# Kernel optimization log

Hardware: AMD Instinct MI355X
Metric: run time of the kernel (lower is better)

Reference implementation:

```python
import jax, jax.numpy as jnp
import numpy as np

B, C, L = 8, 512, 4096
KC, VC, H = 512, 512, 8
DK, DV = KC // H, VC // H
EPS = 1e-5


def _ln(x, g, b):
    m = jnp.mean(x, axis=-1, keepdims=True)
    v = jnp.var(x, axis=-1, keepdims=True)
    return (x - m) * jax.lax.rsqrt(v + EPS) * g + b


def setup_inputs() -> dict:
    key = jax.random.key(0)
    ks = jax.random.split(key, 12)
    s = 0.02
    return {
        "z1": jax.random.normal(ks[0], (B, C, L), jnp.float32),
        "z2": jax.random.normal(ks[1], (B, C, L), jnp.float32),
        "Wq": jax.random.normal(ks[2], (KC, C), jnp.float32) * s,
        "bq": jnp.zeros((KC,), jnp.float32),
        "Wk": jax.random.normal(ks[3], (KC, C), jnp.float32) * s,
        "bk": jnp.zeros((KC,), jnp.float32),
        "Wv": jax.random.normal(ks[4], (VC, C), jnp.float32) * s,
        "bv": jnp.zeros((VC,), jnp.float32),
        "Wr": jax.random.normal(ks[5], (C, VC), jnp.float32) * s,
        "br": jnp.zeros((C,), jnp.float32),
        "g1": jnp.ones((C,), jnp.float32),
        "be1": jnp.zeros((C,), jnp.float32),
        "W1": jax.random.normal(ks[6], (2 * C, C), jnp.float32) * s,
        "b1": jnp.zeros((2 * C,), jnp.float32),
        "W2": jax.random.normal(ks[7], (C, 2 * C), jnp.float32) * s,
        "b2": jnp.zeros((C,), jnp.float32),
        "g2": jnp.ones((C,), jnp.float32),
        "be2": jnp.zeros((C,), jnp.float32),
    }


def reference(z1, z2, Wq, bq, Wk, bk, Wv, bv, Wr, br, g1, be1, W1, b1, W2, b2, g2, be2):
    # 1x1 Conv1d projections (channels-first)
    q = jnp.einsum('oc,bcl->bol', Wq, z1) + bq[None, :, None]
    k = jnp.einsum('oc,bcl->bol', Wk, z2) + bk[None, :, None]
    v = jnp.einsum('oc,bcl->bol', Wv, z2) + bv[None, :, None]
    qh = q.reshape(B, H, DK, L)
    kh = k.reshape(B, H, DK, L)
    vh = v.reshape(B, H, DV, L)
    # efficient attention: keys softmax over length, queries over channels
    kh = jax.nn.softmax(kh, axis=-1)
    qh = jax.nn.softmax(qh, axis=2)
    ctx = jnp.einsum('bhkl,bhvl->bhkv', kh, vh)          # [B,H,DK,DV]
    att = jnp.einsum('bhkv,bhkl->bhvl', ctx, qh)          # [B,H,DV,L]
    att = att.reshape(B, VC, L)
    z = jnp.einsum('oc,bcl->bol', Wr, att) + br[None, :, None] + z1  # reprojection + residual
    # b c l -> b l c, LayerNorm, FFN, back
    x = z.transpose(0, 2, 1)
    x = _ln(x, g1, be1)
    h = jax.nn.elu(x @ W1.T + b1)
    y = h @ W2.T + b2
    y = _ln(y, g2, be2)
    return y.transpose(0, 2, 1)
```

## Files before the change

kernel.cpp:

```cpp
#include <hip/hip_runtime.h>
#include <math.h>

#define B_   8
#define C_   512
#define L_   4096
#define H_   8
#define DK_  64
#define C2_  1024

typedef unsigned short ushort;
typedef short     bf16x8_t __attribute__((ext_vector_type(8)));
typedef float     f32x4_t  __attribute__((ext_vector_type(4)));
typedef unsigned short u16x8 __attribute__((ext_vector_type(8)));
typedef unsigned short u16x4 __attribute__((ext_vector_type(4)));

__device__ __forceinline__ float bf2f(ushort u) {
    unsigned int x = ((unsigned int)u) << 16;
    float f; __builtin_memcpy(&f, &x, 4); return f;
}
__device__ __forceinline__ ushort f2bf(float f) {
    unsigned int x; __builtin_memcpy(&x, &f, 4);
    x = (x + 0x7FFFu + ((x >> 16) & 1u)) >> 16;
    return (ushort)x;
}

#define GLOAD_LDS16(gp, lp) \
    __builtin_amdgcn_global_load_lds((const __attribute__((address_space(1))) void*)(gp), \
                                     (__attribute__((address_space(3))) void*)(lp), 16, 0, 0)

__global__ __launch_bounds__(256) void transpose_in(const float* __restrict__ in,
                                                    ushort* __restrict__ out)
{
    const int b = blockIdx.z, c0 = blockIdx.y * 64, l0 = blockIdx.x * 64;
    __shared__ float t[64][65];
    const int tid = threadIdx.x;
    {
        const int c = tid >> 4, l4 = (tid & 15) * 4;
        const float* ip = in + ((size_t)b * C_ + c0) * L_ + l0;
#pragma unroll
        for (int cc = c; cc < 64; cc += 16) {
            float4 v = *(const float4*)(ip + (size_t)cc * L_ + l4);
            t[l4 + 0][cc] = v.x; t[l4 + 1][cc] = v.y;
            t[l4 + 2][cc] = v.z; t[l4 + 3][cc] = v.w;
        }
    }
    __syncthreads();
    {
        const int l = tid >> 3, c8 = (tid & 7) * 8;
        ushort* op = out + ((size_t)b * L_ + l0) * C_ + c0;
#pragma unroll
        for (int ll = l; ll < 64; ll += 32) {
            u16x8 v;
#pragma unroll
            for (int i = 0; i < 8; ++i) v[i] = f2bf(t[ll][c8 + i]);
            *(u16x8*)(op + (size_t)ll * C_ + c8) = v;
        }
    }
}

__global__ __launch_bounds__(256) void transpose_out(const float* __restrict__ in,
                                                     float* __restrict__ out)
{
    const int b = blockIdx.z, c0 = blockIdx.y * 64, l0 = blockIdx.x * 64;
    __shared__ float t[64][65];
    const int tid = threadIdx.x;
    {
        const int l = tid >> 4, c4 = (tid & 15) * 4;
#pragma unroll
        for (int ll = l; ll < 64; ll += 16) {
            float4 v = *(const float4*)(in + ((size_t)(b * L_ + l0 + ll)) * C_ + c0 + c4);
            t[c4 + 0][ll] = v.x; t[c4 + 1][ll] = v.y;
            t[c4 + 2][ll] = v.z; t[c4 + 3][ll] = v.w;
        }
    }
    __syncthreads();
    {
        const int c = tid >> 4, l4 = (tid & 15) * 4;
        float* op = out + ((size_t)b * C_ + c0) * L_ + l0;
#pragma unroll
        for (int cc = c; cc < 64; cc += 16) {
            float4 v = {t[cc][l4], t[cc][l4 + 1], t[cc][l4 + 2], t[cc][l4 + 3]};
            *(float4*)(op + (size_t)cc * L_ + l4) = v;
        }
    }
}

__global__ __launch_bounds__(256) void cvt_bf16(const float* __restrict__ in,
                                                ushort* __restrict__ out, int n4)
{
    const int i = blockIdx.x * 256 + threadIdx.x;
    if (i < n4) {
        float4 v = *(const float4*)(in + 4 * (size_t)i);
        u16x4 o; o[0] = f2bf(v.x); o[1] = f2bf(v.y); o[2] = f2bf(v.z); o[3] = f2bf(v.w);
        *(u16x4*)(out + 4 * (size_t)i) = o;
    }
}

__global__ __launch_bounds__(256) void zero_kernel(float* __restrict__ p, int n4)
{
    const int i = blockIdx.x * 256 + threadIdx.x;
    if (i < n4) { float4 z = {0.f, 0.f, 0.f, 0.f}; *(float4*)(p + 4 * (size_t)i) = z; }
}

template<int ACT, bool HAS_RES>
__global__ __launch_bounds__(512, 2) void conv_mfma(
    const ushort* __restrict__ A, const ushort* __restrict__ Wt,
    const float* __restrict__ bias, const ushort* __restrict__ res,
    ushort* __restrict__ out, int M, int N, int K)
{
    const int m0 = blockIdx.x * 256;
    const int n0 = blockIdx.y * 256;
    const int tid = threadIdx.x;
    const int w = tid >> 6, lane = tid & 63;
    const int wm = (w >> 2) * 128, wn = (w & 3) * 64;
    const int l16 = lane & 15, quad = lane >> 4;

    __shared__ ushort smem[32768];

    const int sRow = tid >> 2;
    const int sSwz = ((tid & 3) ^ (sRow & 3)) * 8;
    const ushort* gA0 = A  + (size_t)(m0 + sRow) * K + sSwz;
    const ushort* gA1 = A  + (size_t)(m0 + 128 + sRow) * K + sSwz;
    const ushort* gB0 = Wt + (size_t)(n0 + sRow) * K + sSwz;
    const ushort* gB1 = Wt + (size_t)(n0 + 128 + sRow) * K + sSwz;
    const int dA0 = (w * 16) * 32;
    const int dA1 = (128 + w * 16) * 32;

    f32x4_t acc[8][4];
#pragma unroll
    for (int i = 0; i < 8; ++i)
#pragma unroll
        for (int j = 0; j < 4; ++j) acc[i][j] = (f32x4_t){0.f, 0.f, 0.f, 0.f};

    const int nt = K >> 5;

    {
        ushort* bufA = smem;
        ushort* bufB = smem + 8192;
        GLOAD_LDS16(gA0, bufA + dA0);
        GLOAD_LDS16(gA1, bufA + dA1);
        GLOAD_LDS16(gB0, bufB + dA0);
        GLOAD_LDS16(gB1, bufB + dA1);
    }

    for (int t = 0; t < nt; ++t) {
        const ushort* bufA = smem + (t & 1) * 16384;
        const ushort* bufB = bufA + 8192;
        __builtin_amdgcn_s_barrier();
        asm volatile("" ::: "memory");
        if (t + 1 < nt) {
            ushort* nA = smem + ((t + 1) & 1) * 16384;
            ushort* nB = nA + 8192;
            const size_t co = (size_t)(t + 1) * 32;
            GLOAD_LDS16(gA0 + co, nA + dA0);
            GLOAD_LDS16(gA1 + co, nA + dA1);
            GLOAD_LDS16(gB0 + co, nB + dA0);
            GLOAD_LDS16(gB1 + co, nB + dA1);
            asm volatile("s_waitcnt vmcnt(4)" ::: "memory");
        } else {
            asm volatile("s_waitcnt vmcnt(0)" ::: "memory");
        }
        __builtin_amdgcn_s_barrier();
        asm volatile("" ::: "memory");

        bf16x8_t wf[4];
#pragma unroll
        for (int j = 0; j < 4; ++j) {
            const int br = wn + j * 16 + l16;
            wf[j] = *(const bf16x8_t*)(bufB + br * 32 + (quad ^ (br & 3)) * 8);
        }
        __builtin_amdgcn_s_setprio(1);
#pragma unroll
        for (int i = 0; i < 8; ++i) {
            const int ar = wm + i * 16 + l16;
            const bf16x8_t af = *(const bf16x8_t*)(bufA + ar * 32 + (quad ^ (ar & 3)) * 8);
#pragma unroll
            for (int j = 0; j < 4; ++j)
                acc[i][j] = __builtin_amdgcn_mfma_f32_16x16x32_bf16(wf[j], af, acc[i][j], 0, 0, 0);
        }
        __builtin_amdgcn_s_setprio(0);
    }

#pragma unroll
    for (int j = 0; j < 4; ++j) {
        const int nb = n0 + wn + j * 16 + quad * 4;
        const float4 bo = *(const float4*)(bias + nb);
        const float bv[4] = {bo.x, bo.y, bo.z, bo.w};
#pragma unroll
        for (int i = 0; i < 8; ++i) {
            const int m = m0 + wm + i * 16 + l16;
            float v[4];
#pragma unroll
            for (int r = 0; r < 4; ++r) v[r] = acc[i][j][r] + bv[r];
            if (HAS_RES) {
                const u16x4 rv = *(const u16x4*)(res + (size_t)m * N + nb);
#pragma unroll
                for (int r = 0; r < 4; ++r) v[r] += bf2f(rv[r]);
            }
            if (ACT == 1) {
#pragma unroll
                for (int r = 0; r < 4; ++r) v[r] = (v[r] > 0.f) ? v[r] : (__expf(v[r]) - 1.f);
            }
            u16x4 pv;
#pragma unroll
            for (int r = 0; r < 4; ++r) pv[r] = f2bf(v[r]);
            *(u16x4*)(out + (size_t)m * N + nb) = pv;
        }
    }
}

__global__ __launch_bounds__(256) void kstat_chunk(const ushort* __restrict__ k,
                                                   float2* __restrict__ stats)
{
    const int cg = blockIdx.x;
    const int bc = blockIdx.y;
    const int b = bc >> 3, ch = bc & 7;
    const int tid = threadIdx.x;
    const int g = tid & 7;
    const int kk = tid >> 3;
    const int w = tid >> 6, lane = tid & 63;
    const ushort* base = k + ((size_t)(b * L_) + ch * 512) * C_ + cg * 64 + g * 8;

    __shared__ float red[4][8][8];
    __shared__ float mcol[64];

    float fm[8];
#pragma unroll
    for (int i = 0; i < 8; ++i) fm[i] = -3.0e38f;
    for (int r = kk; r < 512; r += 32) {
        u16x8 v = *(const u16x8*)(base + (size_t)r * C_);
#pragma unroll
        for (int i = 0; i < 8; ++i) fm[i] = fmaxf(fm[i], bf2f(v[i]));
    }
#pragma unroll
    for (int off = 8; off <= 32; off <<= 1)
#pragma unroll
        for (int i = 0; i < 8; ++i) fm[i] = fmaxf(fm[i], __shfl_xor(fm[i], off));
    if ((lane >> 3) == 0)
#pragma unroll
        for (int i = 0; i < 8; ++i) red[w][g][i] = fm[i];
    __syncthreads();
    if (tid < 64) {
        const int g2 = tid >> 3, j = tid & 7;
        mcol[g2 * 8 + j] = fmaxf(fmaxf(red[0][g2][j], red[1][g2][j]),
                                 fmaxf(red[2][g2][j], red[3][g2][j]));
    }
    __syncthreads();
    float fmc[8];
#pragma unroll
    for (int i = 0; i < 8; ++i) fmc[i] = mcol[g * 8 + i];

    float fs[8] = {};
    for (int r = kk; r < 512; r += 32) {
        u16x8 v = *(const u16x8*)(base + (size_t)r * C_);
#pragma unroll
        for (int i = 0; i < 8; ++i) fs[i] += __expf(bf2f(v[i]) - fmc[i]);
    }
#pragma unroll
    for (int off = 8; off <= 32; off <<= 1)
#pragma unroll
        for (int i = 0; i < 8; ++i) fs[i] += __shfl_xor(fs[i], off);
    __syncthreads();
    if ((lane >> 3) == 0)
#pragma unroll
        for (int i = 0; i < 8; ++i) red[w][g][i] = fs[i];
    __syncthreads();
    if (tid < 64) {
        const int g2 = tid >> 3, j = tid & 7;
        const float s = red[0][g2][j] + red[1][g2][j] + red[2][g2][j] + red[3][g2][j];
        const int c = cg * 64 + g2 * 8 + j;
        stats[((size_t)(b * C_ + c)) * 8 + ch] = make_float2(mcol[g2 * 8 + j], s);
    }
}

__global__ __launch_bounds__(256) void kstat_merge(const float2* __restrict__ stats,
                                                   float2* __restrict__ minv)
{
    const int i = blockIdx.x * 256 + threadIdx.x;
    if (i >= B_ * C_) return;
    float2 st[8];
    float m = -3.0e38f;
#pragma unroll
    for (int ch = 0; ch < 8; ++ch) { st[ch] = stats[(size_t)i * 8 + ch]; m = fmaxf(m, st[ch].x); }
    float s = 0.f;
#pragma unroll
    for (int ch = 0; ch < 8; ++ch) s += st[ch].y * __expf(st[ch].x - m);
    minv[i] = make_float2(m, 1.f / s);
}

__global__ __launch_bounds__(256) void ctx_mfma(
    const ushort* __restrict__ kk, const ushort* __restrict__ vv,
    const float2* __restrict__ minv, float* __restrict__ ctx)
{
    const int bh = blockIdx.y, b = bh >> 3, h = bh & 7;
    const int l0 = blockIdx.x * 256;
    const int tid = threadIdx.x, w = tid >> 6, lane = tid & 63;
    const int l16 = lane & 15, quad = lane >> 4;

    __shared__ ushort sK[64 * 72];
    __shared__ ushort sV[64 * 72];

    const int grp = tid >> 7;
    const int st  = tid & 127;
    const int sc8 = (st & 7) * 8;
    const int sl4 = (st >> 3) * 4;
    const ushort* gsrc = (grp ? vv : kk)
        + ((size_t)(b * L_ + l0 + sl4)) * C_ + h * 64 + sc8;
    ushort* dst = grp ? sV : sK;

    float2 cst[8];
#pragma unroll
    for (int i = 0; i < 8; ++i)
        cst[i] = minv[(size_t)b * C_ + h * 64 + sc8 + i];

    f32x4_t acc[4];
#pragma unroll
    for (int j = 0; j < 4; ++j) acc[j] = (f32x4_t){0.f, 0.f, 0.f, 0.f};

    for (int tile = 0; tile < 4; ++tile) {
        u16x8 vr[4];
#pragma unroll
        for (int j = 0; j < 4; ++j)
            vr[j] = *(const u16x8*)(gsrc + ((size_t)(tile * 64 + j)) * C_);
        __syncthreads();
        if (grp == 0) {
#pragma unroll
            for (int c = 0; c < 8; ++c) {
                u16x4 o;
#pragma unroll
                for (int j = 0; j < 4; ++j)
                    o[j] = f2bf(__expf(bf2f(vr[j][c]) - cst[c].x) * cst[c].y);
                *(u16x4*)(dst + (sc8 + c) * 72 + sl4) = o;
            }
        } else {
#pragma unroll
            for (int c = 0; c < 8; ++c) {
                u16x4 o;
#pragma unroll
                for (int j = 0; j < 4; ++j) o[j] = vr[j][c];
                *(u16x4*)(dst + (sc8 + c) * 72 + sl4) = o;
            }
        }
        __syncthreads();
#pragma unroll
        for (int k0 = 0; k0 < 64; k0 += 32) {
            const bf16x8_t vf = *(const bf16x8_t*)(sV + (w * 16 + l16) * 72 + k0 + quad * 8);
#pragma unroll
            for (int j = 0; j < 4; ++j) {
                const bf16x8_t kf = *(const bf16x8_t*)(sK + (j * 16 + l16) * 72 + k0 + quad * 8);
                acc[j] = __builtin_amdgcn_mfma_f32_16x16x32_bf16(vf, kf, acc[j], 0, 0, 0);
            }
        }
    }
    float* cp = ctx + (size_t)bh * 4096;
#pragma unroll
    for (int j = 0; j < 4; ++j)
#pragma unroll
        for (int r = 0; r < 4; ++r)
            atomicAdd(&cp[(w * 16 + quad * 4 + r) * 64 + (j * 16 + l16)], acc[j][r]);
}

__global__ __launch_bounds__(256) void att_mfma(
    const ushort* __restrict__ q, const float* __restrict__ ctx,
    ushort* __restrict__ att)
{
    const int bh = blockIdx.y, b = bh >> 3, h = bh & 7;
    const int l0 = blockIdx.x * 128;
    const int tid = threadIdx.x, w = tid >> 6, lane = tid & 63;
    const int l16 = lane & 15, quad = lane >> 4;

    __shared__ ushort sQ[128 * 72];
    __shared__ ushort sC[64 * 72];

    {
        const int part = tid & 7;
#pragma unroll
        for (int rr = tid >> 3; rr < 128; rr += 32) {
            u16x8 v = *(const u16x8*)(q + ((size_t)(b * L_ + l0 + rr)) * C_ + h * 64 + part * 8);
            float f[8], m = -3.0e38f;
#pragma unroll
            for (int i = 0; i < 8; ++i) { f[i] = bf2f(v[i]); m = fmaxf(m, f[i]); }
            m = fmaxf(m, __shfl_xor(m, 1));
            m = fmaxf(m, __shfl_xor(m, 2));
            m = fmaxf(m, __shfl_xor(m, 4));
            float s = 0.f;
#pragma unroll
            for (int i = 0; i < 8; ++i) { f[i] = __expf(f[i] - m); s += f[i]; }
            s += __shfl_xor(s, 1); s += __shfl_xor(s, 2); s += __shfl_xor(s, 4);
            const float inv = 1.f / s;
            u16x8 o;
#pragma unroll
            for (int i = 0; i < 8; ++i) o[i] = f2bf(f[i] * inv);
            *(u16x8*)(sQ + rr * 72 + part * 8) = o;
        }
        const int dv = tid >> 2, dk0 = (tid & 3) * 16;
        const float* cp = ctx + (size_t)bh * 4096 + dv * 64 + dk0;
#pragma unroll
        for (int i = 0; i < 16; ++i) sC[dv * 72 + dk0 + i] = f2bf(cp[i]);
    }
    __syncthreads();

    f32x4_t acc[2][4];
#pragma unroll
    for (int i = 0; i < 2; ++i)
#pragma unroll
        for (int j = 0; j < 4; ++j) acc[i][j] = (f32x4_t){0.f, 0.f, 0.f, 0.f};

#pragma unroll
    for (int ks = 0; ks < 2; ++ks) {
        const int k0 = ks * 32;
        bf16x8_t aq[2], bc[4];
#pragma unroll
        for (int i = 0; i < 2; ++i)
            aq[i] = *(const bf16x8_t*)(sQ + (w * 32 + i * 16 + l16) * 72 + k0 + quad * 8);
#pragma unroll
        for (int j = 0; j < 4; ++j)
            bc[j] = *(const bf16x8_t*)(sC + (j * 16 + l16) * 72 + k0 + quad * 8);
#pragma unroll
        for (int i = 0; i < 2; ++i)
#pragma unroll
            for (int j = 0; j < 4; ++j)
                acc[i][j] = __builtin_amdgcn_mfma_f32_16x16x32_bf16(aq[i], bc[j], acc[i][j], 0, 0, 0);
    }

#pragma unroll
    for (int j = 0; j < 4; ++j)
#pragma unroll
        for (int i = 0; i < 2; ++i) {
            const int mb = l0 + w * 32 + i * 16 + quad * 4;
#pragma unroll
            for (int r = 0; r < 4; ++r)
                att[((size_t)(b * L_ + mb + r)) * C_ + h * 64 + j * 16 + l16] = f2bf(acc[i][j][r]);
        }
}

template<bool OUTF32>
__global__ __launch_bounds__(256) void ln_row(
    const ushort* __restrict__ in, const float* __restrict__ g,
    const float* __restrict__ be, ushort* __restrict__ outb,
    float* __restrict__ outf)
{
    const int tid = threadIdx.x, w = tid >> 6, lane = tid & 63;
    const size_t row = (size_t)blockIdx.x * 4 + w;
    const ushort* p = in + row * C_ + lane * 8;
    u16x8 v = *(const u16x8*)p;
    float f[8], s = 0.f, s2 = 0.f;
#pragma unroll
    for (int i = 0; i < 8; ++i) { f[i] = bf2f(v[i]); s += f[i]; s2 = fmaf(f[i], f[i], s2); }
#pragma unroll
    for (int o = 1; o < 64; o <<= 1) { s += __shfl_xor(s, o); s2 += __shfl_xor(s2, o); }
    const float mean = s * (1.f / C_);
    const float var  = s2 * (1.f / C_) - mean * mean;
    const float inv  = rsqrtf(var + 1e-5f);
    if (OUTF32) {
        float* op = outf + row * C_ + lane * 8;
#pragma unroll
        for (int i = 0; i < 8; ++i)
            op[i] = (f[i] - mean) * inv * g[lane * 8 + i] + be[lane * 8 + i];
    } else {
        u16x8 ov;
#pragma unroll
        for (int i = 0; i < 8; ++i)
            ov[i] = f2bf((f[i] - mean) * inv * g[lane * 8 + i] + be[lane * 8 + i]);
        *(u16x8*)(outb + row * C_ + lane * 8) = ov;
    }
}

extern "C" void kernel_launch(void* const* d_in, const int* in_sizes, int n_in,
                              void* d_out, int out_size, void* d_ws, size_t ws_size,
                              hipStream_t stream)
{
    const float* z1  = (const float*)d_in[0];
    const float* z2  = (const float*)d_in[1];
    const float* Wq  = (const float*)d_in[2];
    const float* bq  = (const float*)d_in[3];
    const float* Wk  = (const float*)d_in[4];
    const float* bk  = (const float*)d_in[5];
    const float* Wv  = (const float*)d_in[6];
    const float* bv  = (const float*)d_in[7];
    const float* Wr  = (const float*)d_in[8];
    const float* br  = (const float*)d_in[9];
    const float* g1  = (const float*)d_in[10];
    const float* be1 = (const float*)d_in[11];
    const float* W1  = (const float*)d_in[12];
    const float* b1  = (const float*)d_in[13];
    const float* W2  = (const float*)d_in[14];
    const float* b2  = (const float*)d_in[15];
    const float* g2  = (const float*)d_in[16];
    const float* be2 = (const float*)d_in[17];
    float* out = (float*)d_out;

    const size_t SB = (size_t)B_ * L_ * C_;
    ushort* ws16 = (ushort*)d_ws;
    ushort* b0v = ws16;
    ushort* b1v = ws16 + SB;
    ushort* b2v = ws16 + 2 * SB;
    ushort* b3v = ws16 + 3 * SB;
    ushort* wb  = ws16 + 4 * SB;
    ushort* wbq = wb;
    ushort* wbk = wb + 262144;
    ushort* wbv = wb + 524288;
    ushort* wbr = wb + 786432;
    ushort* wb1 = wb + 1048576;
    ushort* wb2 = wb + 1572864;
    float*  ctxf = (float*)(wb + 2097152);
    float2* stats = (float2*)(ctxf + 65536);
    float2* minv  = stats + (size_t)B_ * C_ * 8;
    ushort* vbuf = (ushort*)d_out;
    ushort* hbuf = (ushort*)d_out;
    float*  yf32 = (float*)b2v;

    const dim3 blk(256);
    const dim3 blk512(512);
    const int M = B_ * L_;

    transpose_in<<<dim3(L_/64, C_/64, B_), blk, 0, stream>>>(z1, b0v);
    transpose_in<<<dim3(L_/64, C_/64, B_), blk, 0, stream>>>(z2, b1v);
    cvt_bf16<<<dim3(262144/4/256), blk, 0, stream>>>(Wq, wbq, 262144/4);
    cvt_bf16<<<dim3(262144/4/256), blk, 0, stream>>>(Wk, wbk, 262144/4);
    cvt_bf16<<<dim3(262144/4/256), blk, 0, stream>>>(Wv, wbv, 262144/4);
    cvt_bf16<<<dim3(262144/4/256), blk, 0, stream>>>(Wr, wbr, 262144/4);
    cvt_bf16<<<dim3(524288/4/256), blk, 0, stream>>>(W1, wb1, 524288/4);
    cvt_bf16<<<dim3(524288/4/256), blk, 0, stream>>>(W2, wb2, 524288/4);

    conv_mfma<0,false><<<dim3(M/256, C_/256), blk512, 0, stream>>>(b0v, wbq, bq, nullptr, b2v, M, C_, C_);
    conv_mfma<0,false><<<dim3(M/256, C_/256), blk512, 0, stream>>>(b1v, wbk, bk, nullptr, b3v, M, C_, C_);
    conv_mfma<0,false><<<dim3(M/256, C_/256), blk512, 0, stream>>>(b1v, wbv, bv, nullptr, vbuf, M, C_, C_);

    kstat_chunk<<<dim3(C_/64, B_ * 8), blk, 0, stream>>>(b3v, stats);
    kstat_merge<<<dim3((B_ * C_ + 255) / 256), blk, 0, stream>>>(stats, minv);

    zero_kernel<<<dim3(65536/256), blk, 0, stream>>>(ctxf, 65536);
    ctx_mfma<<<dim3(16, B_ * H_), blk, 0, stream>>>(b3v, vbuf, minv, ctxf);

    att_mfma<<<dim3(L_/128, B_ * H_), blk, 0, stream>>>(b2v, ctxf, b1v);

    conv_mfma<0,true><<<dim3(M/256, C_/256), blk512, 0, stream>>>(b1v, wbr, br, b0v, b2v, M, C_, C_);

    ln_row<false><<<dim3(M/4), blk, 0, stream>>>(b2v, g1, be1, b3v, nullptr);

    conv_mfma<1,false><<<dim3(M/256, C2_/256), blk512, 0, stream>>>(b3v, wb1, b1, nullptr, hbuf, M, C2_, C_);

    conv_mfma<0,false><<<dim3(M/256, C_/256), blk512, 0, stream>>>(hbuf, wb2, b2, nullptr, b0v, M, C_, C2_);

    ln_row<true><<<dim3(M/4), blk, 0, stream>>>(b0v, g2, be2, nullptr, yf32);

    transpose_out<<<dim3(L_/64, C_/64, B_), blk, 0, stream>>>(yf32, out);
}
```

Before: 553.5 us.

## Deepen GEMM K-tile to 64 with finer-grained staged prefetch and LDS-staged epilogue

The conv_mfma GEMM now loads 64-wide K tiles into a 128KB double-buffered LDS region, split into four 16-element K slabs. Each slab is prefetched and consumed in its own barrier phase, so loads for the next tile are interleaved with MFMA work on the current one. The LDS layout changes to a 16-element row with XOR half-swizzle. The epilogue stages bf16 results through per-wave LDS tiles so global stores become 16-byte row-contiguous writes. The larger LDS footprint (128KB) likely limits occupancy to one block per CU despite launch_bounds(512,2), and the kernel now has more barriers per tile.

```diff
diff --git a/kernel.cpp b/kernel.cpp
--- a/kernel.cpp
+++ b/kernel.cpp
@@ -112,19 +112,24 @@
     const int n0 = blockIdx.y * 256;
     const int tid = threadIdx.x;
     const int w = tid >> 6, lane = tid & 63;
-    const int wm = (w >> 2) * 128, wn = (w & 3) * 64;
+    const int wm2 = (w >> 2) * 128, wn = (w & 3) * 64;
     const int l16 = lane & 15, quad = lane >> 4;
 
-    __shared__ ushort smem[32768];
-
-    const int sRow = tid >> 2;
-    const int sSwz = ((tid & 3) ^ (sRow & 3)) * 8;
-    const ushort* gA0 = A  + (size_t)(m0 + sRow) * K + sSwz;
-    const ushort* gA1 = A  + (size_t)(m0 + 128 + sRow) * K + sSwz;
-    const ushort* gB0 = Wt + (size_t)(n0 + sRow) * K + sSwz;
-    const ushort* gB1 = Wt + (size_t)(n0 + 128 + sRow) * K + sSwz;
-    const int dA0 = (w * 16) * 32;
-    const int dA1 = (128 + w * 16) * 32;
+    __shared__ ushort smem[65536];
+
+    const int sRow = tid >> 1, sHalf = tid & 1;
+    const int sh = sHalf ^ ((sRow >> 2) & 1);
+    const ushort* gA = A  + (size_t)(m0 + sRow) * K + sh * 8;
+    const ushort* gB = Wt + (size_t)(n0 + sRow) * K + sh * 8;
+    const int ldst = tid * 8;
+
+    const int baseA = wm2 + l16;
+    const int baseB = wn + l16;
+    const int hA = (quad & 1) ^ ((baseA >> 2) & 1);
+    const int hB = (quad & 1) ^ ((baseB >> 2) & 1);
+    const int qhi = (quad >> 1) * 4096;
+    const int aoff = qhi + baseA * 16 + hA * 8;
+    const int boff = qhi + 16384 + baseB * 16 + hB * 8;
 
     f32x4_t acc[8][4];
 #pragma unroll
@@ -132,79 +137,90 @@
 #pragma unroll
         for (int j = 0; j < 4; ++j) acc[i][j] = (f32x4_t){0.f, 0.f, 0.f, 0.f};
 
-    const int nt = K >> 5;
-
-    {
-        ushort* bufA = smem;
-        ushort* bufB = smem + 8192;
-        GLOAD_LDS16(gA0, bufA + dA0);
-        GLOAD_LDS16(gA1, bufA + dA1);
-        GLOAD_LDS16(gB0, bufB + dA0);
-        GLOAD_LDS16(gB1, bufB + dA1);
+    const int nt = K >> 6;
+
+#pragma unroll
+    for (int q = 0; q < 4; ++q) {
+        GLOAD_LDS16(gA + q * 16, smem + q * 4096 + ldst);
+        GLOAD_LDS16(gB + q * 16, smem + 16384 + q * 4096 + ldst);
     }
 
     for (int t = 0; t < nt; ++t) {
-        const ushort* bufA = smem + (t & 1) * 16384;
-        const ushort* bufB = bufA + 8192;
-        __builtin_amdgcn_s_barrier();
-        asm volatile("" ::: "memory");
-        if (t + 1 < nt) {
-            ushort* nA = smem + ((t + 1) & 1) * 16384;
-            ushort* nB = nA + 8192;
-            const size_t co = (size_t)(t + 1) * 32;
-            GLOAD_LDS16(gA0 + co, nA + dA0);
-            GLOAD_LDS16(gA1 + co, nA + dA1);
-            GLOAD_LDS16(gB0 + co, nB + dA0);
-            GLOAD_LDS16(gB1 + co, nB + dA1);
-            asm volatile("s_waitcnt vmcnt(4)" ::: "memory");
-        } else {
-            asm volatile("s_waitcnt vmcnt(0)" ::: "memory");
-        }
-        __builtin_amdgcn_s_barrier();
-        asm volatile("" ::: "memory");
-
-        bf16x8_t wf[4];
+        const int cb = (t & 1) * 32768;
+        const int nb = 32768 - cb;
+        const bool pf = (t + 1 < nt);
+#pragma unroll
+        for (int p = 0; p < 4; ++p) {
+            if (pf) {
+                const int ko = (t + 1) * 64 + p * 16;
+                GLOAD_LDS16(gA + ko, smem + nb + p * 4096 + ldst);
+                GLOAD_LDS16(gB + ko, smem + nb + 16384 + p * 4096 + ldst);
+                asm volatile("s_waitcnt vmcnt(6)" ::: "memory");
+            } else {
+                if (p < 2) { asm volatile("s_waitcnt vmcnt(4)" ::: "memory"); }
+                else       { asm volatile("s_waitcnt vmcnt(0)" ::: "memory"); }
+            }
+            __builtin_amdgcn_s_barrier();
+            asm volatile("" ::: "memory");
+
+            const int ih = p & 1;
+            const ushort* base = smem + cb + (p >> 1) * 8192;
+            bf16x8_t wf[4], af[4];
+#pragma unroll
+            for (int x = 0; x < 4; ++x) {
+                wf[x] = *(const bf16x8_t*)(base + boff + x * 256);
+                af[x] = *(const bf16x8_t*)(base + aoff + (ih * 4 + x) * 256);
+            }
+            __builtin_amdgcn_s_setprio(1);
+#pragma unroll
+            for (int x = 0; x < 4; ++x)
+#pragma unroll
+                for (int j = 0; j < 4; ++j)
+                    acc[ih * 4 + x][j] =
+                        __builtin_amdgcn_mfma_f32_16x16x32_bf16(wf[j], af[x], acc[ih * 4 + x][j], 0, 0, 0);
+            __builtin_amdgcn_s_setprio(0);
+        }
+    }
+
+    __syncthreads();
+    ushort* sT = smem + w * 4608;
+#pragma unroll
+    for (int h2 = 0; h2 < 2; ++h2) {
 #pragma unroll
         for (int j = 0; j < 4; ++j) {
-            const int br = wn + j * 16 + l16;
-            wf[j] = *(const bf16x8_t*)(bufB + br * 32 + (quad ^ (br & 3)) * 8);
-        }
-        __builtin_amdgcn_s_setprio(1);
-#pragma unroll
-        for (int i = 0; i < 8; ++i) {
-            const int ar = wm + i * 16 + l16;
-            const bf16x8_t af = *(const bf16x8_t*)(bufA + ar * 32 + (quad ^ (ar & 3)) * 8);
-#pragma unroll
-            for (int j = 0; j < 4; ++j)
-                acc[i][j] = __builtin_amdgcn_mfma_f32_16x16x32_bf16(wf[j], af, acc[i][j], 0, 0, 0);
-        }
-        __builtin_amdgcn_s_setprio(0);
-    }
-
-#pragma unroll
-    for (int j = 0; j < 4; ++j) {
-        const int nb = n0 + wn + j * 16 + quad * 4;
-        const float4 bo = *(const float4*)(bias + nb);
-        const float bv[4] = {bo.x, bo.y, bo.z, bo.w};
-#pragma unroll
-        for (int i = 0; i < 8; ++i) {
-            const int m = m0 + wm + i * 16 + l16;
-            float v[4];
-#pragma unroll
-            for (int r = 0; r < 4; ++r) v[r] = acc[i][j][r] + bv[r];
-            if (HAS_RES) {
-                const u16x4 rv = *(const u16x4*)(res + (size_t)m * N + nb);
-#pragma unroll
-                for (int r = 0; r < 4; ++r) v[r] += bf2f(rv[r]);
-            }
-            if (ACT == 1) {
-#pragma unroll
-                for (int r = 0; r < 4; ++r) v[r] = (v[r] > 0.f) ? v[r] : (__expf(v[r]) - 1.f);
-            }
-            u16x4 pv;
-#pragma unroll
-            for (int r = 0; r < 4; ++r) pv[r] = f2bf(v[r]);
-            *(u16x4*)(out + (size_t)m * N + nb) = pv;
+            const int nb4 = wn + j * 16 + quad * 4;
+            const float4 bo = *(const float4*)(bias + n0 + nb4);
+            const float bv[4] = {bo.x, bo.y, bo.z, bo.w};
+#pragma unroll
+            for (int x = 0; x < 4; ++x) {
+                const int ml = x * 16 + l16;
+                const int m = m0 + wm2 + h2 * 64 + ml;
+                float v[4];
+#pragma unroll
+                for (int r = 0; r < 4; ++r) v[r] = acc[h2 * 4 + x][j][r] + bv[r];
+                if (HAS_RES) {
+                    const u16x4 rv = *(const u16x4*)(res + (size_t)m * N + n0 + nb4);
+#pragma unroll
+                    for (int r = 0; r < 4; ++r) v[r] += bf2f(rv[r]);
+                }
+                if (ACT == 1) {
+#pragma unroll
+                    for (int r = 0; r < 4; ++r) v[r] = (v[r] > 0.f) ? v[r] : (__expf(v[r]) - 1.f);
+                }
+                u16x4 pv;
+#pragma unroll
+                for (int r = 0; r < 4; ++r) pv[r] = f2bf(v[r]);
+                *(u16x4*)(sT + ml * 72 + (nb4 - wn)) = pv;
+            }
+        }
+        {
+            const int rr = lane >> 3, ch = lane & 7;
+#pragma unroll
+            for (int rep = 0; rep < 8; ++rep) {
+                const int ml = rep * 8 + rr;
+                const u16x8 vo = *(const u16x8*)(sT + ml * 72 + ch * 8);
+                *(u16x8*)(out + (size_t)(m0 + wm2 + h2 * 64 + ml) * N + n0 + wn + ch * 8) = vo;
+            }
         }
     }
 }
```

New measurement: 519.5 us. -6.1%, faster.

## Shrink GEMM M-tile to 128, add LDS-staged coalesced epilogue and XOR swizzle

Applied to the files above, without the earlier changes.

The conv GEMM kernel now uses 128x256 tiles instead of 256x256, halving accumulator registers and raising the occupancy hint to 4 blocks per CU. The LDS swizzle gains an extra XOR term to reduce bank conflicts. Output is staged through shared memory so each wave writes 16-byte coalesced rows instead of scattered 8-byte stores. The pipeline changes from explicit vmcnt waits to __syncthreads after each k-step. This lowers arithmetic intensity per tile and may weaken overlap of loads with compute.

```diff
diff --git a/kernel.cpp b/kernel.cpp
--- a/kernel.cpp
+++ b/kernel.cpp
@@ -103,97 +103,89 @@
 }
 
 template<int ACT, bool HAS_RES>
-__global__ __launch_bounds__(512, 2) void conv_mfma(
+__global__ __launch_bounds__(512, 4) void conv_mfma(
     const ushort* __restrict__ A, const ushort* __restrict__ Wt,
     const float* __restrict__ bias, const ushort* __restrict__ res,
     ushort* __restrict__ out, int M, int N, int K)
 {
-    const int m0 = blockIdx.x * 256;
+    const int m0 = blockIdx.x * 128;
     const int n0 = blockIdx.y * 256;
     const int tid = threadIdx.x;
     const int w = tid >> 6, lane = tid & 63;
-    const int wm = (w >> 2) * 128, wn = (w & 3) * 64;
+    const int wm = (w >> 2) * 64, wn = (w & 3) * 64;
     const int l16 = lane & 15, quad = lane >> 4;
 
-    __shared__ ushort smem[32768];
-
-    const int sRow = tid >> 2;
-    const int sSwz = ((tid & 3) ^ (sRow & 3)) * 8;
-    const ushort* gA0 = A  + (size_t)(m0 + sRow) * K + sSwz;
-    const ushort* gA1 = A  + (size_t)(m0 + 128 + sRow) * K + sSwz;
-    const ushort* gB0 = Wt + (size_t)(n0 + sRow) * K + sSwz;
-    const ushort* gB1 = Wt + (size_t)(n0 + 128 + sRow) * K + sSwz;
-    const int dA0 = (w * 16) * 32;
-    const int dA1 = (128 + w * 16) * 32;
-
-    f32x4_t acc[8][4];
-#pragma unroll
-    for (int i = 0; i < 8; ++i)
+    __shared__ ushort smem[36864];
+
+    const int rowA = tid >> 2, slotA = tid & 3;
+    const int gsA = slotA ^ (rowA & 3) ^ ((rowA >> 2) & 3);
+    const ushort* gA = A + (size_t)(m0 + rowA) * K + gsA * 8;
+    const int rowB0 = tid >> 2, rowB1 = 128 + (tid >> 2), slotB = tid & 3;
+    const int gsB0 = slotB ^ (rowB0 & 3) ^ ((rowB0 >> 2) & 3);
+    const int gsB1 = slotB ^ (rowB1 & 3) ^ ((rowB1 >> 2) & 3);
+    const ushort* gB0 = Wt + (size_t)(n0 + rowB0) * K + gsB0 * 8;
+    const ushort* gB1 = Wt + (size_t)(n0 + rowB1) * K + gsB1 * 8;
+
+    f32x4_t acc[4][4];
+#pragma unroll
+    for (int i = 0; i < 4; ++i)
 #pragma unroll
         for (int j = 0; j < 4; ++j) acc[i][j] = (f32x4_t){0.f, 0.f, 0.f, 0.f};
 
     const int nt = K >> 5;
 
-    {
-        ushort* bufA = smem;
-        ushort* bufB = smem + 8192;
-        GLOAD_LDS16(gA0, bufA + dA0);
-        GLOAD_LDS16(gA1, bufA + dA1);
-        GLOAD_LDS16(gB0, bufB + dA0);
-        GLOAD_LDS16(gB1, bufB + dA1);
-    }
+#define STAGE_T(ko_, boff_) do { \
+        GLOAD_LDS16(gA + (ko_), smem + (boff_) + tid * 8); \
+        GLOAD_LDS16(gB0 + (ko_), smem + (boff_) + 4096 + tid * 8); \
+        GLOAD_LDS16(gB1 + (ko_), smem + (boff_) + 8192 + tid * 8); \
+    } while (0)
+
+    STAGE_T(0, 0);
+    __syncthreads();
 
     for (int t = 0; t < nt; ++t) {
-        const ushort* bufA = smem + (t & 1) * 16384;
-        const ushort* bufB = bufA + 8192;
-        __builtin_amdgcn_s_barrier();
-        asm volatile("" ::: "memory");
-        if (t + 1 < nt) {
-            ushort* nA = smem + ((t + 1) & 1) * 16384;
-            ushort* nB = nA + 8192;
-            const size_t co = (size_t)(t + 1) * 32;
-            GLOAD_LDS16(gA0 + co, nA + dA0);
-            GLOAD_LDS16(gA1 + co, nA + dA1);
-            GLOAD_LDS16(gB0 + co, nB + dA0);
-            GLOAD_LDS16(gB1 + co, nB + dA1);
-            asm volatile("s_waitcnt vmcnt(4)" ::: "memory");
-        } else {
-            asm volatile("s_waitcnt vmcnt(0)" ::: "memory");
-        }
-        __builtin_amdgcn_s_barrier();
-        asm volatile("" ::: "memory");
-
+        const int cb = (t & 1) * 12288;
+        if (t + 1 < nt) STAGE_T((t + 1) * 32, 12288 - cb);
+
+        const ushort* bA = smem + cb;
+        const ushort* bB = bA + 4096;
         bf16x8_t wf[4];
 #pragma unroll
         for (int j = 0; j < 4; ++j) {
-            const int br = wn + j * 16 + l16;
-            wf[j] = *(const bf16x8_t*)(bufB + br * 32 + (quad ^ (br & 3)) * 8);
+            const int rw = wn + j * 16 + l16;
+            const int pw = quad ^ (rw & 3) ^ ((rw >> 2) & 3);
+            wf[j] = *(const bf16x8_t*)(bB + rw * 32 + pw * 8);
         }
         __builtin_amdgcn_s_setprio(1);
 #pragma unroll
-        for (int i = 0; i < 8; ++i) {
-            const int ar = wm + i * 16 + l16;
-            const bf16x8_t af = *(const bf16x8_t*)(bufA + ar * 32 + (quad ^ (ar & 3)) * 8);
+        for (int i = 0; i < 4; ++i) {
+            const int ra = wm + i * 16 + l16;
+            const int pa = quad ^ (ra & 3) ^ ((ra >> 2) & 3);
+            const bf16x8_t af = *(const bf16x8_t*)(bA + ra * 32 + pa * 8);
 #pragma unroll
             for (int j = 0; j < 4; ++j)
                 acc[i][j] = __builtin_amdgcn_mfma_f32_16x16x32_bf16(wf[j], af, acc[i][j], 0, 0, 0);
         }
         __builtin_amdgcn_s_setprio(0);
-    }
-
+        __syncthreads();
+    }
+#undef STAGE_T
+
+    ushort* sT = smem + w * 4608;
 #pragma unroll
     for (int j = 0; j < 4; ++j) {
-        const int nb = n0 + wn + j * 16 + quad * 4;
-        const float4 bo = *(const float4*)(bias + nb);
+        const int nb4 = wn + j * 16 + quad * 4;
+        const float4 bo = *(const float4*)(bias + n0 + nb4);
         const float bv[4] = {bo.x, bo.y, bo.z, bo.w};
 #pragma unroll
-        for (int i = 0; i < 8; ++i) {
-            const int m = m0 + wm + i * 16 + l16;
+        for (int i = 0; i < 4; ++i) {
+            const int ml = i * 16 + l16;
+            const int m = m0 + wm + ml;
             float v[4];
 #pragma unroll
             for (int r = 0; r < 4; ++r) v[r] = acc[i][j][r] + bv[r];
             if (HAS_RES) {
-                const u16x4 rv = *(const u16x4*)(res + (size_t)m * N + nb);
+                const u16x4 rv = *(const u16x4*)(res + (size_t)m * N + n0 + nb4);
 #pragma unroll
                 for (int r = 0; r < 4; ++r) v[r] += bf2f(rv[r]);
             }
@@ -204,7 +196,16 @@
             u16x4 pv;
 #pragma unroll
             for (int r = 0; r < 4; ++r) pv[r] = f2bf(v[r]);
-            *(u16x4*)(out + (size_t)m * N + nb) = pv;
+            *(u16x4*)(sT + ml * 72 + (nb4 - wn)) = pv;
+        }
+    }
+    {
+        const int rr = lane >> 3, ch = lane & 7;
+#pragma unroll
+        for (int rep = 0; rep < 8; ++rep) {
+            const int ml = rep * 8 + rr;
+            const u16x8 vo = *(const u16x8*)(sT + ml * 72 + ch * 8);
+            *(u16x8*)(out + (size_t)(m0 + wm + ml) * N + n0 + wn + ch * 8) = vo;
         }
     }
 }
@@ -523,9 +524,9 @@
     cvt_bf16<<<dim3(524288/4/256), blk, 0, stream>>>(W1, wb1, 524288/4);
     cvt_bf16<<<dim3(524288/4/256), blk, 0, stream>>>(W2, wb2, 524288/4);
 
-    conv_mfma<0,false><<<dim3(M/256, C_/256), blk512, 0, stream>>>(b0v, wbq, bq, nullptr, b2v, M, C_, C_);
-    conv_mfma<0,false><<<dim3(M/256, C_/256), blk512, 0, stream>>>(b1v, wbk, bk, nullptr, b3v, M, C_, C_);
-    conv_mfma<0,false><<<dim3(M/256, C_/256), blk512, 0, stream>>>(b1v, wbv, bv, nullptr, vbuf, M, C_, C_);
+    conv_mfma<0,false><<<dim3(M/128, C_/256), blk512, 0, stream>>>(b0v, wbq, bq, nullptr, b2v, M, C_, C_);
+    conv_mfma<0,false><<<dim3(M/128, C_/256), blk512, 0, stream>>>(b1v, wbk, bk, nullptr, b3v, M, C_, C_);
+    conv_mfma<0,false><<<dim3(M/128, C_/256), blk512, 0, stream>>>(b1v, wbv, bv, nullptr, vbuf, M, C_, C_);
 
     kstat_chunk<<<dim3(C_/64, B_ * 8), blk, 0, stream>>>(b3v, stats);
     kstat_merge<<<dim3((B_ * C_ + 255) / 256), blk, 0, stream>>>(stats, minv);
@@ -535,13 +536,13 @@
 
     att_mfma<<<dim3(L_/128, B_ * H_), blk, 0, stream>>>(b2v, ctxf, b1v);
 
-    conv_mfma<0,true><<<dim3(M/256, C_/256), blk512, 0, stream>>>(b1v, wbr, br, b0v, b2v, M, C_, C_);
+    conv_mfma<0,true><<<dim3(M/128, C_/256), blk512, 0, stream>>>(b1v, wbr, br, b0v, b2v, M, C_, C_);
 
     ln_row<false><<<dim3(M/4), blk, 0, stream>>>(b2v, g1, be1, b3v, nullptr);
 
-    conv_mfma<1,false><<<dim3(M/256, C2_/256), blk512, 0, stream>>>(b3v, wb1, b1, nullptr, hbuf, M, C2_, C_);
-
-    conv_mfma<0,false><<<dim3(M/256, C_/256), blk512, 0, stream>>>(hbuf, wb2, b2, nullptr, b0v, M, C_, C2_);
+    conv_mfma<1,false><<<dim3(M/128, C2_/256), blk512, 0, stream>>>(b3v, wb1, b1, nullptr, hbuf, M, C2_, C_);
+
+    conv_mfma<0,false><<<dim3(M/128, C_/256), blk512, 0, stream>>>(hbuf, wb2, b2, nullptr, b0v, M, C_, C2_);
 
     ln_row<true><<<dim3(M/4), blk, 0, stream>>>(b0v, g2, be2, nullptr, yf32);
 
```

New measurement: 506.5 us. 1.09x faster.
